# Kernel tuning notes

Hardware: AMD Instinct MI355X
Metric: run time of the kernel (lower is better)

## Reference

```python
import jax, jax.numpy as jnp
import numpy as np

S, N, CM, CZ, H, D = 512, 768, 64, 128, 8, 32
EPS = 1e-5


def _layer_norm(x, w, b):
    mu = jnp.mean(x, axis=-1, keepdims=True)
    xc = x - mu
    var = jnp.mean(xc * xc, axis=-1, keepdims=True)
    return xc * jax.lax.rsqrt(var + EPS) * w + b


def setup_inputs() -> dict:
    key = jax.random.key(0)
    ks = jax.random.split(key, 6)
    scale_m = 1.0 / np.sqrt(CM)
    scale_z = 1.0 / np.sqrt(CZ)
    scale_o = 1.0 / np.sqrt(H * D)
    return {
        "m": jax.random.normal(ks[0], (1, S, N, CM), jnp.float32),
        "z": jax.random.normal(ks[1], (1, N, N, CZ), jnp.float32),
        "norm_m_w": jnp.ones((CM,), jnp.float32),
        "norm_m_b": jnp.zeros((CM,), jnp.float32),
        "norm_z_w": jnp.ones((CZ,), jnp.float32),
        "norm_z_b": jnp.zeros((CZ,), jnp.float32),
        "wm": jax.random.normal(ks[2], (CM, H * D), jnp.float32) * scale_m,
        "wg": jax.random.normal(ks[3], (CM, H * D), jnp.float32) * scale_m,
        "wz": jax.random.normal(ks[4], (CZ, H), jnp.float32) * scale_z,
        "wo": jax.random.normal(ks[5], (H * D, CM), jnp.float32) * scale_o,
    }


def reference(m, z, norm_m_w, norm_m_b, norm_z_w, norm_z_b, wm, wg, wz, wo):
    m0 = m[0]  # [S, N, CM]
    z0 = z[0]  # [N, N, CZ]
    mn = _layer_norm(m0, norm_m_w, norm_m_b)
    zn = _layer_norm(z0, norm_z_w, norm_z_b)
    # b[p,q,h]; original code softmaxes over the LAST axis of b'[h,p,q] (axis q)
    # but contracts as o[s,q] = sum_p w[p,q] v[s,p] (transpose_a matmul),
    # so softmax is over axis q = axis 1 of [p,q,h].
    b = jnp.einsum('pqc,ch->pqh', zn, wz)
    w = jax.nn.softmax(b, axis=1)  # normalized over q for each p (faithful to source)
    v = jnp.einsum('spc,ck->spk', mn, wm).reshape(S, N, H, D)
    g = jax.nn.sigmoid(jnp.einsum('spc,ck->spk', mn, wg)).reshape(S, N, H, D)
    o = jnp.einsum('pqh,sphd->sqhd', w, v) * g  # weighted average then gate
    out = jnp.einsum('sqhd,hdc->sqc', o, wo.reshape(H, D, CM))
    return out[None]  # [1, S, N, CM]
```

## Files before the change

kernel.cpp:

```cpp
#include <hip/hip_runtime.h>
#include <hip/hip_bf16.h>
#include <stdint.h>

#define S_DIM 512
#define N_DIM 768
#define CMd   64
#define CZd   128
#define Hd    8
#define Dd    32
#define HDd   256

typedef float          f32x4  __attribute__((ext_vector_type(4)));
typedef __bf16         bf16x8 __attribute__((ext_vector_type(8)));
typedef unsigned int   u32x4  __attribute__((ext_vector_type(4)));
typedef unsigned int   u32x2  __attribute__((ext_vector_type(2)));
typedef unsigned short u16x8  __attribute__((ext_vector_type(8)));

__device__ __forceinline__ unsigned short f2bf(float f) {
  __bf16 h = (__bf16)f;
  return __builtin_bit_cast(unsigned short, h);
}
__device__ __forceinline__ float bf2f(unsigned short u) {
  unsigned int x = ((unsigned int)u) << 16;
  return __builtin_bit_cast(float, x);
}
__device__ __forceinline__ float sigmoidf_(float x) {
  return 1.f / (1.f + __expf(-x));
}

__global__ __launch_bounds__(256) void k0_prep(const float* __restrict__ wm,
                                               const float* __restrict__ wg,
                                               const float* __restrict__ wo,
                                               unsigned short* __restrict__ WBT,
                                               unsigned short* __restrict__ woT) {
  int t = blockIdx.x * 256 + threadIdx.x;
  if (t < 512 * 64) {
    int j = t >> 6, c = t & 63;
    float v = (j < 256) ? wm[c * 256 + j] : wg[c * 256 + (j - 256)];
    WBT[t] = f2bf(v);
  }
  if (t < 64 * 256) {
    int c = t >> 8, k = t & 255;
    woT[t] = f2bf(wo[k * 64 + c]);
  }
}

__global__ __launch_bounds__(256) void k1_zln_b(const float* __restrict__ z,
                                                const float* __restrict__ nzw,
                                                const float* __restrict__ nzb,
                                                const float* __restrict__ wz,
                                                float* __restrict__ b_e) {
  __shared__ float wzT[8][128];
  int t = threadIdx.x;
  for (int i = t; i < 1024; i += 256) {
    int h = i >> 7, c = i & 127;
    wzT[h][c] = wz[c * 8 + h];
  }
  __syncthreads();

  int lane = t & 63, w = t >> 6;
  int sub = lane & 7;
  int rloc = lane >> 3;
  int p = blockIdx.y;
  int q = blockIdx.x * 32 + w * 8 + rloc;

  const float* zr = z + ((size_t)p * N_DIM + q) * CZd + sub * 16;
  f32x4 v[4];
#pragma unroll
  for (int j = 0; j < 4; j++) v[j] = *(const f32x4*)(zr + 4 * j);

  float s1 = 0.f, s2 = 0.f;
#pragma unroll
  for (int j = 0; j < 4; j++)
#pragma unroll
    for (int e = 0; e < 4; e++) { float x = v[j][e]; s1 += x; s2 += x * x; }
  s1 += __shfl_xor(s1, 1); s2 += __shfl_xor(s2, 1);
  s1 += __shfl_xor(s1, 2); s2 += __shfl_xor(s2, 2);
  s1 += __shfl_xor(s1, 4); s2 += __shfl_xor(s2, 4);
  float mean = s1 * (1.f / 128.f);
  float var  = s2 * (1.f / 128.f) - mean * mean;
  float rstd = rsqrtf(var + 1e-5f);

  const float* wp = nzw + sub * 16;
  const float* bp = nzb + sub * 16;
  float zn[16];
#pragma unroll
  for (int j = 0; j < 4; j++) {
    f32x4 wv = *(const f32x4*)(wp + 4 * j);
    f32x4 bv = *(const f32x4*)(bp + 4 * j);
#pragma unroll
    for (int e = 0; e < 4; e++)
      zn[j * 4 + e] = (v[j][e] - mean) * rstd * wv[e] + bv[e];
  }

  float accb[8];
#pragma unroll
  for (int h = 0; h < 8; h++) {
    const f32x4* wr = (const f32x4*)&wzT[h][sub * 16];
    float a = 0.f;
#pragma unroll
    for (int j = 0; j < 4; j++) {
      f32x4 ww = wr[j];
#pragma unroll
      for (int e = 0; e < 4; e++) a += zn[j * 4 + e] * ww[e];
    }
    accb[h] = a;
  }
#pragma unroll
  for (int mask = 1; mask <= 4; mask <<= 1)
#pragma unroll
    for (int h = 0; h < 8; h++) accb[h] += __shfl_xor(accb[h], mask);

  float outv = accb[0];
#pragma unroll
  for (int h = 1; h < 8; h++) outv = (sub == h) ? accb[h] : outv;
  b_e[((size_t)p * 8 + sub) * 768 + q] = outv;
}

__global__ __launch_bounds__(256) void k1b_softmax(float* __restrict__ b_e,
                                                   float* __restrict__ invs) {
  int row = blockIdx.x;
  int t = threadIdx.x;
  float* base = b_e + (size_t)row * 768;
  float x0 = base[t], x1 = base[t + 256], x2 = base[t + 512];
  __shared__ float red[256];
  red[t] = fmaxf(x0, fmaxf(x1, x2));
  __syncthreads();
  for (int o = 128; o > 0; o >>= 1) {
    if (t < o) red[t] = fmaxf(red[t], red[t + o]);
    __syncthreads();
  }
  float M = red[0];
  __syncthreads();
  float e0 = __expf(x0 - M), e1 = __expf(x1 - M), e2 = __expf(x2 - M);
  base[t] = e0; base[t + 256] = e1; base[t + 512] = e2;
  red[t] = e0 + e1 + e2;
  __syncthreads();
  for (int o = 128; o > 0; o >>= 1) {
    if (t < o) red[t] += red[t + o];
    __syncthreads();
  }
  if (t == 0) invs[row] = 1.0f / red[0];
}

__global__ __launch_bounds__(256) void k1b2_transpose(const float* __restrict__ b_e,
                                                      const float* __restrict__ invs,
                                                      unsigned short* __restrict__ Aw) {
  int t = threadIdx.x;
  int q0 = blockIdx.x * 64, p0 = blockIdx.y * 64, h = blockIdx.z;
  __shared__ unsigned short T[64][65];
  int i = t >> 2, ch = t & 3;
  size_t rowid = (size_t)(p0 + i) * 8 + h;
  const float* src = b_e + rowid * 768 + q0 + ch * 16;
  float inv = invs[rowid];
#pragma unroll
  for (int jj = 0; jj < 16; jj += 4) {
    f32x4 v = *(const f32x4*)(src + jj);
#pragma unroll
    for (int e = 0; e < 4; e++) T[i][ch * 16 + jj + e] = f2bf(v[e] * inv);
  }
  __syncthreads();
  int j = i;
  unsigned short outv[16];
#pragma unroll
  for (int ii = 0; ii < 16; ii++) outv[ii] = T[ch * 16 + ii][j];
  unsigned short* dst = Aw + ((size_t)h * 768 + q0 + j) * 768 + p0 + ch * 16;
  *(u32x4*)(dst)     = *(u32x4*)(outv);
  *(u32x4*)(dst + 8) = *(u32x4*)(outv + 8);
}

__global__ __launch_bounds__(256) void k2_mln_vg(const float* __restrict__ mp,
                                                 const float* __restrict__ nmw,
                                                 const float* __restrict__ nmb,
                                                 const unsigned short* __restrict__ WBT,
                                                 unsigned short* __restrict__ VT,
                                                 unsigned short* __restrict__ G) {
  __shared__ unsigned short WBs[512 * 64];
  __shared__ unsigned short As[64 * 64];
  int t = threadIdx.x;
  int p0 = blockIdx.x * 64;

#pragma unroll
  for (int it = 0; it < 16; it++) {
    int cid = t + it * 256;
    int row = cid >> 3, ch = cid & 7;
    u32x4 v = *(const u32x4*)(WBT + row * 64 + ch * 8);
    *(u32x4*)(WBs + row * 64 + ((ch * 8) ^ ((row & 7) << 3))) = v;
  }

  int lane = t & 63, w = t >> 6;
  int n0 = w * 128;
  int lr = lane & 15, lk8 = (lane >> 4) * 8;
  f32x4 zero = {0.f, 0.f, 0.f, 0.f};

#pragma unroll 1
  for (int si = 0; si < 4; si++) {
    int s = blockIdx.y * 4 + si;

    {
      int row = t >> 2, qt = t & 3;
      const float* mr = mp + ((size_t)s * N_DIM + p0 + row) * CMd + qt * 16;
      f32x4 v[4];
#pragma unroll
      for (int j = 0; j < 4; j++) v[j] = *(const f32x4*)(mr + 4 * j);
      float s1 = 0.f, s2 = 0.f;
#pragma unroll
      for (int j = 0; j < 4; j++)
#pragma unroll
        for (int e = 0; e < 4; e++) { float x = v[j][e]; s1 += x; s2 += x * x; }
      s1 += __shfl_xor(s1, 1); s2 += __shfl_xor(s2, 1);
      s1 += __shfl_xor(s1, 2); s2 += __shfl_xor(s2, 2);
      float mean = s1 * (1.f / 64.f);
      float var  = s2 * (1.f / 64.f) - mean * mean;
      float rstd = rsqrtf(var + 1e-5f);
      unsigned short o[16];
#pragma unroll
      for (int j = 0; j < 4; j++) {
        f32x4 wv = *(const f32x4*)(nmw + qt * 16 + 4 * j);
        f32x4 bv = *(const f32x4*)(nmb + qt * 16 + 4 * j);
#pragma unroll
        for (int e = 0; e < 4; e++)
          o[j * 4 + e] = f2bf((v[j][e] - mean) * rstd * wv[e] + bv[e]);
      }
      int k0 = qt * 16;
      *(u32x4*)(As + row * 64 + ((k0) ^ ((row & 7) << 3)))     = *(u32x4*)(o);
      *(u32x4*)(As + row * 64 + ((k0 + 8) ^ ((row & 7) << 3))) = *(u32x4*)(o + 8);
    }
    __syncthreads();

    f32x4 acc[4][8];
#pragma unroll
    for (int i = 0; i < 4; i++)
#pragma unroll
      for (int j = 0; j < 8; j++) acc[i][j] = zero;

#pragma unroll
    for (int kk = 0; kk < 2; kk++) {
      bf16x8 bfr[8];
#pragma unroll
      for (int nt = 0; nt < 8; nt++) {
        int r = n0 + nt * 16 + lr;
        bfr[nt] = *(const bf16x8*)(WBs + r * 64 + ((kk * 32 + lk8) ^ ((r & 7) << 3)));
      }
#pragma unroll
      for (int mt = 0; mt < 4; mt++) {
        int ar = mt * 16 + lr;
        bf16x8 a = *(const bf16x8*)(As + ar * 64 + ((kk * 32 + lk8) ^ ((ar & 7) << 3)));
#pragma unroll
        for (int nt = 0; nt < 8; nt++)
          acc[mt][nt] = __builtin_amdgcn_mfma_f32_16x16x32_bf16(a, bfr[nt], acc[mt][nt], 0, 0, 0);
      }
    }

#pragma unroll
    for (int mt = 0; mt < 4; mt++)
#pragma unroll
      for (int nt = 0; nt < 8; nt++) {
        int j = n0 + nt * 16 + lr;
        int ploc = mt * 16 + (lane >> 4) * 4;
        if (j < 256) {
          int h = j >> 5, d = j & 31;
          unsigned short pk[4];
#pragma unroll
          for (int r = 0; r < 4; r++) pk[r] = f2bf(acc[mt][nt][r]);
          *(u32x2*)(VT + ((size_t)h * 16384 + s * 32 + d) * 768 + p0 + ploc) = *(u32x2*)pk;
        } else {
          int jj = j - 256;
#pragma unroll
          for (int r = 0; r < 4; r++)
            G[((size_t)s * 768 + p0 + ploc + r) * 256 + jj] = f2bf(sigmoidf_(acc[mt][nt][r]));
        }
      }
    __syncthreads();
  }
}

__global__ __launch_bounds__(256) void k3_gemm(const unsigned short* __restrict__ Aw,
                                               const unsigned short* __restrict__ VT,
                                               unsigned short* __restrict__ O) {
  __shared__ unsigned short Asl[128 * 64];
  __shared__ unsigned short Bsl[128 * 64];
  int t = threadIdx.x;
  int flat = blockIdx.x;
  int h = blockIdx.y;
  int f2 = (flat & 7) * 96 + (flat >> 3);
  int mt_b = f2 % 6, nt_b = f2 / 6;
  int q0 = mt_b * 128, n0 = nt_b * 128;

  const unsigned short* Ab = Aw + (size_t)h * 768 * 768 + (size_t)q0 * 768;
  const unsigned short* Bb = VT + (size_t)h * 16384 * 768 + (size_t)n0 * 768;

  int lane = t & 63, w = t >> 6;
  int wr = (w >> 1) * 64, wc = (w & 1) * 64;
  int lr = lane & 15, lk8 = (lane >> 4) * 8;
  int ch = t & 7, r0 = t >> 3;

  u32x4 ra[4], rb[4];
#pragma unroll
  for (int it = 0; it < 4; it++) {
    int r = r0 + it * 32;
    ra[it] = *(const u32x4*)(Ab + (size_t)r * 768 + ch * 8);
    rb[it] = *(const u32x4*)(Bb + (size_t)r * 768 + ch * 8);
  }

  f32x4 zero = {0.f, 0.f, 0.f, 0.f};
  f32x4 acc[4][4];
#pragma unroll
  for (int i = 0; i < 4; i++)
#pragma unroll
    for (int j = 0; j < 4; j++) acc[i][j] = zero;

  for (int kt = 0; kt < 12; kt++) {
#pragma unroll
    for (int it = 0; it < 4; it++) {
      int cid = t + it * 256;
      int row = cid >> 3, c = cid & 7;
      int idx = row * 64 + ((c * 8) ^ ((row & 7) << 3));
      *(u32x4*)(Asl + idx) = ra[it];
      *(u32x4*)(Bsl + idx) = rb[it];
    }
    __syncthreads();
    if (kt < 11) {
      int k0 = (kt + 1) * 64;
#pragma unroll
      for (int it = 0; it < 4; it++) {
        int r = r0 + it * 32;
        ra[it] = *(const u32x4*)(Ab + (size_t)r * 768 + k0 + ch * 8);
        rb[it] = *(const u32x4*)(Bb + (size_t)r * 768 + k0 + ch * 8);
      }
    }
#pragma unroll
    for (int kk = 0; kk < 2; kk++) {
      bf16x8 afr[4], bfr[4];
#pragma unroll
      for (int i = 0; i < 4; i++) {
        int arr = wr + i * 16 + lr;
        int brr = wc + i * 16 + lr;
        afr[i] = *(const bf16x8*)(Asl + arr * 64 + ((kk * 32 + lk8) ^ ((arr & 7) << 3)));
        bfr[i] = *(const bf16x8*)(Bsl + brr * 64 + ((kk * 32 + lk8) ^ ((brr & 7) << 3)));
      }
#pragma unroll
      for (int mt = 0; mt < 4; mt++)
#pragma unroll
        for (int nt = 0; nt < 4; nt++)
          acc[mt][nt] = __builtin_amdgcn_mfma_f32_16x16x32_bf16(afr[mt], bfr[nt], acc[mt][nt], 0, 0, 0);
    }
    __syncthreads();
  }

#pragma unroll
  for (int mt = 0; mt < 4; mt++)
#pragma unroll
    for (int nt = 0; nt < 4; nt++) {
      int q = q0 + wr + mt * 16 + (lane >> 4) * 4;
      int n = n0 + wc + nt * 16 + lr;
      int s_ = n >> 5, d = n & 31;
      size_t ob = ((size_t)s_ * 768 + q) * 256 + h * 32 + d;
#pragma unroll
      for (int r = 0; r < 4; r++)
        O[ob + (size_t)r * 256] = f2bf(acc[mt][nt][r]);
    }
}

__global__ __launch_bounds__(256) void k4_out(const unsigned short* __restrict__ O,
                                              const unsigned short* __restrict__ G,
                                              const unsigned short* __restrict__ woT,
                                              float* __restrict__ out) {
  __shared__ unsigned short OGs[64 * 256];
  __shared__ unsigned short WOs[64 * 256];
  int t = threadIdx.x;
  int q0 = blockIdx.x * 64;

#pragma unroll
  for (int it = 0; it < 8; it++) {
    int cid = t + it * 256;
    int row = cid >> 5, ch = cid & 31;
    u32x4 v = *(const u32x4*)(woT + row * 256 + ch * 8);
    *(u32x4*)(WOs + row * 256 + ((ch * 8) ^ ((row & 7) << 3))) = v;
  }

  int lane = t & 63, w = t >> 6;
  int lr = lane & 15, lk8 = (lane >> 4) * 8;
  f32x4 zero = {0.f, 0.f, 0.f, 0.f};
  int i = t >> 2, c4 = t & 3;

#pragma unroll 1
  for (int si = 0; si < 4; si++) {
    int s = blockIdx.y * 4 + si;

    const unsigned short* Orow = O + ((size_t)s * 768 + q0 + i) * 256 + c4 * 64;
    const unsigned short* Grow = G + ((size_t)s * 768 + q0 + i) * 256 + c4 * 64;
#pragma unroll
    for (int jj = 0; jj < 8; jj++) {
      u16x8 ov = *(const u16x8*)(Orow + jj * 8);
      u16x8 gv = *(const u16x8*)(Grow + jj * 8);
      unsigned short pk[8];
#pragma unroll
      for (int e = 0; e < 8; e++) pk[e] = f2bf(bf2f(ov[e]) * bf2f(gv[e]));
      *(u32x4*)(OGs + i * 256 + ((c4 * 64 + jj * 8) ^ ((i & 7) << 3))) = *(u32x4*)pk;
    }
    __syncthreads();

    f32x4 acc[4];
#pragma unroll
    for (int nt = 0; nt < 4; nt++) acc[nt] = zero;

#pragma unroll
    for (int kk = 0; kk < 8; kk++) {
      int ar = w * 16 + lr;
      bf16x8 a = *(const bf16x8*)(OGs + ar * 256 + ((kk * 32 + lk8) ^ ((ar & 7) << 3)));
#pragma unroll
      for (int nt = 0; nt < 4; nt++) {
        int br = nt * 16 + lr;
        bf16x8 b = *(const bf16x8*)(WOs + br * 256 + ((kk * 32 + lk8) ^ ((br & 7) << 3)));
        acc[nt] = __builtin_amdgcn_mfma_f32_16x16x32_bf16(a, b, acc[nt], 0, 0, 0);
      }
    }

#pragma unroll
    for (int nt = 0; nt < 4; nt++) {
      int q = q0 + w * 16 + (lane >> 4) * 4;
      int c = nt * 16 + lr;
      float* dst = out + ((size_t)s * 768 + q) * 64 + c;
#pragma unroll
      for (int r = 0; r < 4; r++) dst[(size_t)r * 64] = acc[nt][r];
    }
    __syncthreads();
  }
}

extern "C" void kernel_launch(void* const* d_in, const int* in_sizes, int n_in,
                              void* d_out, int out_size, void* d_ws, size_t ws_size,
                              hipStream_t stream) {
  const float* m   = (const float*)d_in[0];
  const float* z   = (const float*)d_in[1];
  const float* nmw = (const float*)d_in[2];
  const float* nmb = (const float*)d_in[3];
  const float* nzw = (const float*)d_in[4];
  const float* nzb = (const float*)d_in[5];
  const float* wm  = (const float*)d_in[6];
  const float* wg  = (const float*)d_in[7];
  const float* wz  = (const float*)d_in[8];
  const float* wo  = (const float*)d_in[9];
  float* out = (float*)d_out;

  char* ws = (char*)d_ws;
  size_t off = 0;
  auto alloc = [&](size_t bytes) -> void* {
    void* p = ws + off;
    off += (bytes + 1023) & ~(size_t)1023;
    return p;
  };
  float*          b_e  = (float*)alloc((size_t)768 * 8 * 768 * 4);
  float*          invs = (float*)alloc((size_t)768 * 8 * 4);
  unsigned short* Awt  = (unsigned short*)alloc((size_t)8 * 768 * 768 * 2);
  unsigned short* WBT  = (unsigned short*)alloc((size_t)512 * 64 * 2);
  unsigned short* woT  = (unsigned short*)alloc((size_t)64 * 256 * 2);
  unsigned short* VT   = (unsigned short*)alloc((size_t)8 * 16384 * 768 * 2);
  unsigned short* G    = (unsigned short*)alloc((size_t)512 * 768 * 256 * 2);
  unsigned short* O    = (unsigned short*)alloc((size_t)512 * 768 * 256 * 2);
  if (ws_size < off) return;

  k0_prep<<<128, 256, 0, stream>>>(wm, wg, wo, WBT, woT);
  k1_zln_b<<<dim3(24, 768), 256, 0, stream>>>(z, nzw, nzb, wz, b_e);
  k1b_softmax<<<6144, 256, 0, stream>>>(b_e, invs);
  k1b2_transpose<<<dim3(12, 12, 8), 256, 0, stream>>>(b_e, invs, Awt);
  k2_mln_vg<<<dim3(12, 128), 256, 0, stream>>>(m, nmw, nmb, WBT, VT, G);
  k3_gemm<<<dim3(768, 8), 256, 0, stream>>>(Awt, VT, O);
  k4_out<<<dim3(12, 128), 256, 0, stream>>>(O, G, woT, out);
}
```

Measured before the change: 675.0 us.

## Defer softmax exp to transpose, double-buffer GEMM prefetch, halve k2/k4 grids

The softmax kernel no longer writes the exponentials back. It stores the per-row max, and the transpose kernel recomputes exp(x-M)*inv, which removes a full write pass over b_e. The attention GEMM now keeps two register stages of global prefetch, loading two k-tiles ahead to hide more load latency, at the cost of more registers per thread. k2 and k4 each handle 8 sequence rows per block instead of 4, halving their grids so the resident weight tiles are reused more, though fewer blocks may reduce occupancy.

```diff
diff --git a/kernel.cpp b/kernel.cpp
--- a/kernel.cpp
+++ b/kernel.cpp
@@ -117,11 +117,12 @@
   b_e[((size_t)p * 8 + sub) * 768 + q] = outv;
 }
 
-__global__ __launch_bounds__(256) void k1b_softmax(float* __restrict__ b_e,
+__global__ __launch_bounds__(256) void k1b_softmax(const float* __restrict__ b_e,
+                                                   float* __restrict__ Ms,
                                                    float* __restrict__ invs) {
   int row = blockIdx.x;
   int t = threadIdx.x;
-  float* base = b_e + (size_t)row * 768;
+  const float* base = b_e + (size_t)row * 768;
   float x0 = base[t], x1 = base[t + 256], x2 = base[t + 512];
   __shared__ float red[256];
   red[t] = fmaxf(x0, fmaxf(x1, x2));
@@ -133,17 +134,17 @@
   float M = red[0];
   __syncthreads();
   float e0 = __expf(x0 - M), e1 = __expf(x1 - M), e2 = __expf(x2 - M);
-  base[t] = e0; base[t + 256] = e1; base[t + 512] = e2;
   red[t] = e0 + e1 + e2;
   __syncthreads();
   for (int o = 128; o > 0; o >>= 1) {
     if (t < o) red[t] += red[t + o];
     __syncthreads();
   }
-  if (t == 0) invs[row] = 1.0f / red[0];
+  if (t == 0) { Ms[row] = M; invs[row] = 1.0f / red[0]; }
 }
 
 __global__ __launch_bounds__(256) void k1b2_transpose(const float* __restrict__ b_e,
+                                                      const float* __restrict__ Ms,
                                                       const float* __restrict__ invs,
                                                       unsigned short* __restrict__ Aw) {
   int t = threadIdx.x;
@@ -152,12 +153,14 @@
   int i = t >> 2, ch = t & 3;
   size_t rowid = (size_t)(p0 + i) * 8 + h;
   const float* src = b_e + rowid * 768 + q0 + ch * 16;
+  float M = Ms[rowid];
   float inv = invs[rowid];
 #pragma unroll
   for (int jj = 0; jj < 16; jj += 4) {
     f32x4 v = *(const f32x4*)(src + jj);
 #pragma unroll
-    for (int e = 0; e < 4; e++) T[i][ch * 16 + jj + e] = f2bf(v[e] * inv);
+    for (int e = 0; e < 4; e++)
+      T[i][ch * 16 + jj + e] = f2bf(__expf(v[e] - M) * inv);
   }
   __syncthreads();
   int j = i;
@@ -194,8 +197,8 @@
   f32x4 zero = {0.f, 0.f, 0.f, 0.f};
 
 #pragma unroll 1
-  for (int si = 0; si < 4; si++) {
-    int s = blockIdx.y * 4 + si;
+  for (int si = 0; si < 8; si++) {
+    int s = blockIdx.y * 8 + si;
 
     {
       int row = t >> 2, qt = t & 3;
@@ -295,13 +298,15 @@
   int lr = lane & 15, lk8 = (lane >> 4) * 8;
   int ch = t & 7, r0 = t >> 3;
 
-  u32x4 ra[4], rb[4];
-#pragma unroll
-  for (int it = 0; it < 4; it++) {
-    int r = r0 + it * 32;
-    ra[it] = *(const u32x4*)(Ab + (size_t)r * 768 + ch * 8);
-    rb[it] = *(const u32x4*)(Bb + (size_t)r * 768 + ch * 8);
-  }
+  u32x4 ra[2][4], rb[2][4];
+#pragma unroll
+  for (int b = 0; b < 2; b++)
+#pragma unroll
+    for (int it = 0; it < 4; it++) {
+      int r = r0 + it * 32;
+      ra[b][it] = *(const u32x4*)(Ab + (size_t)r * 768 + b * 64 + ch * 8);
+      rb[b][it] = *(const u32x4*)(Bb + (size_t)r * 768 + b * 64 + ch * 8);
+    }
 
   f32x4 zero = {0.f, 0.f, 0.f, 0.f};
   f32x4 acc[4][4];
@@ -311,22 +316,23 @@
     for (int j = 0; j < 4; j++) acc[i][j] = zero;
 
   for (int kt = 0; kt < 12; kt++) {
+    int cur = kt & 1;
 #pragma unroll
     for (int it = 0; it < 4; it++) {
       int cid = t + it * 256;
       int row = cid >> 3, c = cid & 7;
       int idx = row * 64 + ((c * 8) ^ ((row & 7) << 3));
-      *(u32x4*)(Asl + idx) = ra[it];
-      *(u32x4*)(Bsl + idx) = rb[it];
-    }
-    __syncthreads();
-    if (kt < 11) {
-      int k0 = (kt + 1) * 64;
+      *(u32x4*)(Asl + idx) = ra[cur][it];
+      *(u32x4*)(Bsl + idx) = rb[cur][it];
+    }
+    __syncthreads();
+    if (kt < 10) {
+      int k0 = (kt + 2) * 64;
 #pragma unroll
       for (int it = 0; it < 4; it++) {
         int r = r0 + it * 32;
-        ra[it] = *(const u32x4*)(Ab + (size_t)r * 768 + k0 + ch * 8);
-        rb[it] = *(const u32x4*)(Bb + (size_t)r * 768 + k0 + ch * 8);
+        ra[cur][it] = *(const u32x4*)(Ab + (size_t)r * 768 + k0 + ch * 8);
+        rb[cur][it] = *(const u32x4*)(Bb + (size_t)r * 768 + k0 + ch * 8);
       }
     }
 #pragma unroll
@@ -385,8 +391,8 @@
   int i = t >> 2, c4 = t & 3;
 
 #pragma unroll 1
-  for (int si = 0; si < 4; si++) {
-    int s = blockIdx.y * 4 + si;
+  for (int si = 0; si < 8; si++) {
+    int s = blockIdx.y * 8 + si;
 
     const unsigned short* Orow = O + ((size_t)s * 768 + q0 + i) * 256 + c4 * 64;
     const unsigned short* Grow = G + ((size_t)s * 768 + q0 + i) * 256 + c4 * 64;
@@ -452,6 +458,7 @@
     return p;
   };
   float*          b_e  = (float*)alloc((size_t)768 * 8 * 768 * 4);
+  float*          Ms   = (float*)alloc((size_t)768 * 8 * 4);
   float*          invs = (float*)alloc((size_t)768 * 8 * 4);
   unsigned short* Awt  = (unsigned short*)alloc((size_t)8 * 768 * 768 * 2);
   unsigned short* WBT  = (unsigned short*)alloc((size_t)512 * 64 * 2);
@@ -463,9 +470,9 @@
 
   k0_prep<<<128, 256, 0, stream>>>(wm, wg, wo, WBT, woT);
   k1_zln_b<<<dim3(24, 768), 256, 0, stream>>>(z, nzw, nzb, wz, b_e);
-  k1b_softmax<<<6144, 256, 0, stream>>>(b_e, invs);
-  k1b2_transpose<<<dim3(12, 12, 8), 256, 0, stream>>>(b_e, invs, Awt);
-  k2_mln_vg<<<dim3(12, 128), 256, 0, stream>>>(m, nmw, nmb, WBT, VT, G);
+  k1b_softmax<<<6144, 256, 0, stream>>>(b_e, Ms, invs);
+  k1b2_transpose<<<dim3(12, 12, 8), 256, 0, stream>>>(b_e, Ms, invs, Awt);
+  k2_mln_vg<<<dim3(12, 64), 256, 0, stream>>>(m, nmw, nmb, WBT, VT, G);
   k3_gemm<<<dim3(768, 8), 256, 0, stream>>>(Awt, VT, O);
-  k4_out<<<dim3(12, 128), 256, 0, stream>>>(O, G, woT, out);
-}
+  k4_out<<<dim3(12, 64), 256, 0, stream>>>(O, G, woT, out);
+}
```

Result: slower. 704.0 us (+4.3%).
